# Performance work log

Hardware: AMD Instinct MI355X
Metric: run time of the kernel (lower is better)

Reference implementation:

```python
import jax, jax.numpy as jnp
import numpy as np

N, E, R, D = 50000, 640000, 200, 128  # nodes, edges, relations, feat dim (in_feat==out_feat)
EPS = 1e-5  # LayerNorm eps
NEG_SLOPE = 0.01  # F.leaky_relu default

def _xavier(k, shape):
    gain = np.sqrt(2.0)  # calculate_gain('relu')
    std = gain * np.sqrt(2.0 / (shape[0] + shape[1]))
    a = np.sqrt(3.0) * std
    return jax.random.uniform(k, shape, jnp.float32, -a, a)

def setup_inputs() -> dict:
    key = jax.random.key(0)
    ks = jax.random.split(key, 10)
    return {
        "node": jax.random.normal(ks[0], (N, D), jnp.float32),
        "rel": jax.random.normal(ks[1], (R, D), jnp.float32),
        "norm": jax.random.uniform(ks[2], (N, 1), jnp.float32),
        "w_triplet": _xavier(ks[3], (3 * D, D)),
        "w_quad": _xavier(ks[4], (D, D)),
        "loop_weight": _xavier(ks[5], (D, D)),
        "evolve_loop_weight": _xavier(ks[6], (D, D)),
        "src": jax.random.randint(ks[7], (E,), 0, N),
        "dst": jax.random.randint(ks[8], (E,), 0, N),
        "etype": jax.random.randint(ks[9], (E,), 0, R),
    }

def reference(node, rel, norm, w_triplet, w_quad, loop_weight, evolve_loop_weight, src, dst, etype):
    # triplet = cat([h_src, rel_emb, h_dst], 1) @ w_triplet, computed blockwise
    # to avoid materializing the [E, 3D] concat.
    W_s, W_r, W_d = w_triplet[:D], w_triplet[D:2 * D], w_triplet[2 * D:]
    triplet = node[src] @ W_s + rel[etype] @ W_r + node[dst] @ W_d  # [E, D]
    # 'fre' not in edata -> sro_fre is zeros; a_triplet = triplet @ w_quad
    a = jax.nn.leaky_relu(triplet @ w_quad, negative_slope=NEG_SLOPE)  # [E, D]
    # edge_softmax: softmax over incoming edges per destination node, per feature
    a_max = jax.ops.segment_max(a, dst, num_segments=N)
    a_max = jnp.where(jnp.isfinite(a_max), a_max, 0.0)  # empty segments -> -inf
    ex = jnp.exp(a - a_max[dst])
    denom = jax.ops.segment_sum(ex, dst, num_segments=N)
    att = ex / denom[dst]
    # weighted scatter-sum aggregation, then apply_func: h * norm
    h = jax.ops.segment_sum(att * triplet, dst, num_segments=N) * norm  # [N, D]
    # self-loop: evolve_loop_weight for in-degree-0 nodes, loop_weight otherwise
    indeg = jax.ops.segment_sum(jnp.ones((E,), jnp.float32), dst, num_segments=N)
    loop = jnp.where((indeg > 0)[:, None], node @ loop_weight, node @ evolve_loop_weight)
    out = h + loop
    # LayerNorm(elementwise_affine=False)
    mu = jnp.mean(out, axis=-1, keepdims=True)
    var = jnp.var(out, axis=-1, keepdims=True)
    return (out - mu) * jax.lax.rsqrt(var + EPS)
```

## Files before the change

kernel.cpp:

```cpp
#include <hip/hip_runtime.h>
#include <hip/hip_bf16.h>

#define D 128

typedef __attribute__((ext_vector_type(8))) short bf16x8;
typedef __attribute__((ext_vector_type(4))) float f32x4;

__device__ __forceinline__ unsigned short f2bf_bits(float f) {
    union { __hip_bfloat16 h; unsigned short u; } c;
    c.h = __float2bfloat16(f);
    return c.u;
}
__device__ __forceinline__ float bfbits2f(unsigned short u) {
    return __uint_as_float(((unsigned)u) << 16);
}
__device__ __forceinline__ float ldf(const void* p, size_t i, int f32) {
    return f32 ? ((const float*)p)[i] : bfbits2f(((const unsigned short*)p)[i]);
}
__device__ __forceinline__ void unpk(unsigned u, float& a, float& b) {
    a = __uint_as_float(u << 16);
    b = __uint_as_float(u & 0xFFFF0000u);
}

__global__ __launch_bounds__(256) void prep_kernel(
    const void* __restrict__ node, const void* __restrict__ wtrip,
    const void* __restrict__ wquad, const void* __restrict__ loopW,
    const void* __restrict__ evoW, unsigned short* __restrict__ wT,
    int* __restrict__ cnt, const int* __restrict__ dst, int* __restrict__ flag,
    int E) {
    __shared__ int sflag;
    int tid = threadIdx.x;
    int bad = 0;
    if (tid < 64) {
        for (int j = 0; j < 4; j++) {
            float v = bfbits2f(((const unsigned short*)node)[tid + 64 * j]);
            if (!(fabsf(v) < 1e4f)) bad = 1;
        }
    }
    unsigned long long m = __ballot(bad);
    if (tid == 0) sflag = (m != 0ull) ? 1 : 0;
    __syncthreads();
    int f32 = sflag;
    int bx = blockIdx.x;
    if (bx == 0 && tid == 0) *flag = f32;

    if (bx < 192) {
        int unit = bx * 2 + (tid >> 7);
        int k = unit & 127, mjob = unit >> 7;
        int t = tid & 127;
        float acc = 0.f;
        for (int j = 0; j < D; j++)
            acc += ldf(wtrip, (size_t)mjob * D * D + (size_t)k * D + j, f32) *
                   ldf(wquad, (size_t)j * D + t, f32);
        const int jmap0 = (mjob == 0) ? 0 : (mjob == 1 ? 6 : 2);
        wT[(size_t)jmap0 * D * D + (size_t)t * D + k] = f2bf_bits(acc);
    } else if (bx < 272) {
        int u = bx - 192;
        int jr = u >> 4, seg = u & 15;
        const void* srcp; size_t base; int j;
        switch (jr) {
            case 0: srcp = wtrip; base = 0;             j = 1; break;
            case 1: srcp = wtrip; base = 2 * D * D;     j = 3; break;
            case 2: srcp = loopW; base = 0;             j = 4; break;
            case 3: srcp = evoW;  base = 0;             j = 5; break;
            default: srcp = wtrip; base = (size_t)D * D; j = 7; break;
        }
        for (int c = tid; c < 1024; c += 256) {
            int idx = seg * 1024 + c;
            int n = idx >> 7, k = idx & 127;
            unsigned short b = f32 ? f2bf_bits(((const float*)srcp)[base + (size_t)k * D + n])
                                   : ((const unsigned short*)srcp)[base + (size_t)k * D + n];
            wT[(size_t)j * D * D + (size_t)n * D + k] = b;
        }
    } else {
        int e = (bx - 272) * 256 + tid;
        if (e < E) atomicAdd(&cnt[dst[e]], 1);
    }
}

__global__ void scan_block(const int* __restrict__ cnt, int* __restrict__ offs,
                           int* __restrict__ part, int N) {
    __shared__ int sh[256];
    int tid = threadIdx.x;
    int i = blockIdx.x * 256 + tid;
    int v = (i < N) ? cnt[i] : 0;
    sh[tid] = v;
    __syncthreads();
    for (int o = 1; o < 256; o <<= 1) {
        int t = (tid >= o) ? sh[tid - o] : 0;
        __syncthreads();
        sh[tid] += t;
        __syncthreads();
    }
    if (i < N) offs[i] = sh[tid] - v;
    if (tid == 255) part[blockIdx.x] = sh[255];
}

__global__ void scan_fix(int* __restrict__ offs, const int* __restrict__ part,
                         int N, int E) {
    __shared__ int sh[256];
    int tid = threadIdx.x, b = blockIdx.x;
    sh[tid] = (tid < b) ? part[tid] : 0;
    __syncthreads();
    for (int o = 128; o; o >>= 1) {
        if (tid < o) sh[tid] += sh[tid + o];
        __syncthreads();
    }
    int carry = sh[0];
    int i = b * 256 + tid;
    if (i < N) offs[i] += carry;
    if (b == 0 && tid == 0) offs[N] = E;
}

__global__ __launch_bounds__(256) void gemm_kernel(
    const void* __restrict__ node, const void* __restrict__ rel,
    const unsigned short* __restrict__ wT, const int* __restrict__ cnt,
    unsigned* __restrict__ nodeST, unsigned* __restrict__ nodeDT,
    unsigned* __restrict__ relRT, unsigned* __restrict__ loopSel,
    const int* __restrict__ flag, int N, int R, int nodeBlocks,
    const int* __restrict__ src, const int* __restrict__ dst,
    const int* __restrict__ et, const int* __restrict__ offs,
    int* __restrict__ cur, unsigned* __restrict__ ePack, int E) {
    __shared__ __align__(16) unsigned short Wt[D][D + 8];

    int bx = blockIdx.x, by = blockIdx.y;
    int tid = threadIdx.y * 64 + threadIdx.x;
    int isRel = 0, jp;
    if (bx >= nodeBlocks) {
        if (by == 1) {
            int e = (bx - nodeBlocks) * 256 + tid;
            if (e < E) {
                int d = dst[e];
                int pos = offs[d] + atomicAdd(&cur[d], 1);
                ePack[pos] = (unsigned)src[e] | ((unsigned)et[e] << 20);
            }
            return;
        }
        if (by != 0 || bx - nodeBlocks >= (R + 63) / 64) return;
        isRel = 1;
        jp = 3;
    } else {
        jp = by;
    }

    int f32 = *flag;
    int rows = isRel ? R : N;
    int row0 = (isRel ? bx - nodeBlocks : bx) * 64;
    const void* A = isRel ? rel : node;

    int lane = threadIdx.x, wv = threadIdx.y;
    int l16 = lane & 15, quad = lane >> 4;
    int ar = row0 + wv * 16 + l16;
    int ar_c = ar < rows ? ar : rows - 1;

    int qIdx, tIdx;
    unsigned* O = nullptr;
    switch (jp) {
        case 0: qIdx = 0; tIdx = 1; O = nodeST; break;
        case 1: qIdx = 2; tIdx = 3; O = nodeDT; break;
        case 2: qIdx = 4; tIdx = 5; break;
        default: qIdx = 6; tIdx = 7; O = relRT; break;
    }

    bf16x8 af[4];
#pragma unroll
    for (int kk = 0; kk < 4; kk++) {
        int k = kk * 32 + quad * 8;
        if (f32) {
            const float* Af = (const float*)A + (size_t)ar_c * D + k;
#pragma unroll
            for (int j = 0; j < 8; j++) af[kk][j] = (short)f2bf_bits(Af[j]);
        } else {
            af[kk] = *(const bf16x8*)((const unsigned short*)A + (size_t)ar_c * D + k);
        }
    }

    const unsigned short* gQ = wT + (size_t)qIdx * D * D;
    const unsigned short* gT = wT + (size_t)tIdx * D * D;

    bf16x8 wreg[8], wreg2[8];
#pragma unroll
    for (int i = 0; i < 8; i++) {
        int c = tid + i * 256;
        wreg[i] = *(const bf16x8*)(gQ + (c >> 4) * 128 + (c & 15) * 8);
    }

    f32x4 accQ[8], accT[8];
#pragma unroll
    for (int i = 0; i < 8; i++) {
        accQ[i] = (f32x4){0.f, 0.f, 0.f, 0.f};
        accT[i] = (f32x4){0.f, 0.f, 0.f, 0.f};
    }

    for (int pass = 0; pass < 2; pass++) {
#pragma unroll
        for (int i = 0; i < 8; i++) {
            int c = tid + i * 256;
            *(bf16x8*)(&Wt[c >> 4][(c & 15) * 8]) = wreg[i];
        }
        if (pass == 0) {
#pragma unroll
            for (int i = 0; i < 8; i++) {
                int c = tid + i * 256;
                wreg2[i] = *(const bf16x8*)(gT + (c >> 4) * 128 + (c & 15) * 8);
            }
        }
        __syncthreads();
        f32x4* acc = pass ? accT : accQ;
#pragma unroll
        for (int kk = 0; kk < 4; kk++) {
#pragma unroll
            for (int nt = 0; nt < 8; nt++) {
                bf16x8 bfr = *(const bf16x8*)(&Wt[nt * 16 + l16][kk * 32 + quad * 8]);
                acc[nt] = __builtin_amdgcn_mfma_f32_16x16x32_bf16(af[kk], bfr, acc[nt], 0, 0, 0);
            }
        }
        __syncthreads();
#pragma unroll
        for (int i = 0; i < 8; i++) wreg[i] = wreg2[i];
    }

    int cr0 = row0 + wv * 16 + quad * 4;
    int odd = l16 & 1;
    if (jp != 2) {
#pragma unroll
        for (int r = 0; r < 4; r++) {
            int cr = cr0 + r;
#pragma unroll
            for (int nt = 0; nt < 8; nt++) {
                float vQ = accQ[nt][r], vT = accT[nt][r];
                float oQ = __shfl_xor(vQ, 1);
                float oT = __shfl_xor(vT, 1);
                unsigned w;
                if (!odd) w = (unsigned)f2bf_bits(vQ) | ((unsigned)f2bf_bits(oQ) << 16);
                else      w = (unsigned)f2bf_bits(oT) | ((unsigned)f2bf_bits(vT) << 16);
                if (cr < rows) O[(size_t)cr * 128 + nt * 16 + l16] = w;
            }
        }
    } else {
#pragma unroll
        for (int r = 0; r < 4; r++) {
            int cr = cr0 + r;
            int deg = (cr < rows) ? cnt[cr] : 0;
#pragma unroll
            for (int nt = 0; nt < 8; nt++) {
                float vL = accQ[nt][r], vE = accT[nt][r];
                float oL = __shfl_xor(vL, 1);
                float oE = __shfl_xor(vE, 1);
                unsigned wl, we;
                if (!odd) {
                    wl = (unsigned)f2bf_bits(vL) | ((unsigned)f2bf_bits(oL) << 16);
                    we = (unsigned)f2bf_bits(vE) | ((unsigned)f2bf_bits(oE) << 16);
                } else {
                    wl = (unsigned)f2bf_bits(oL) | ((unsigned)f2bf_bits(vL) << 16);
                    we = (unsigned)f2bf_bits(oE) | ((unsigned)f2bf_bits(vE) << 16);
                }
                if (cr < rows && !odd)
                    loopSel[(size_t)cr * 64 + nt * 8 + (l16 >> 1)] = (deg > 0) ? wl : we;
            }
        }
    }
}

__global__ __launch_bounds__(256) void agg_kernel(
    const int* __restrict__ offs, const unsigned* __restrict__ ePack,
    const uint2* __restrict__ ST, const uint2* __restrict__ RT,
    const uint2* __restrict__ DT, const unsigned* __restrict__ loopSel,
    const void* __restrict__ normv, void* __restrict__ out,
    const int* __restrict__ flag, int N) {
    int n = blockIdx.x * 4 + threadIdx.y;
    if (n >= N) return;
    int f32 = *flag;
    int lane = threadIdx.x;
    int start = offs[n], end = offs[n + 1];
    int deg = end - start;

    unsigned ul = loopSel[(size_t)n * 64 + lane];
    uint2 ud = DT[(size_t)n * 64 + lane];
    float qd0, qd1, td0, td1, acc0, acc1;
    unpk(ud.x, qd0, qd1);
    unpk(ud.y, td0, td1);
    unpk(ul, acc0, acc1);

    float den0 = 0.f, den1 = 0.f, h0 = 0.f, h1 = 0.f;
    for (int e0 = start; e0 < end; e0 += 64) {
        int m = end - e0;
        if (m > 64) m = 64;
        unsigned pk = (lane < m) ? ePack[e0 + lane] : 0u;
        int j = 0;
#define EDGE_LOADS(J, US, UR)                                         \
        unsigned pk_##US = __shfl(pk, (J));                           \
        uint2 US = ST[(size_t)(pk_##US & 0xFFFFFu) * 64 + lane];      \
        uint2 UR = RT[(size_t)(pk_##US >> 20) * 64 + lane];
#define EDGE_MATH(US, UR)                                             \
        {                                                             \
            float qs0, qs1, qr0, qr1, ts0, ts1, tr0, tr1;             \
            unpk(US.x, qs0, qs1); unpk(UR.x, qr0, qr1);               \
            unpk(US.y, ts0, ts1); unpk(UR.y, tr0, tr1);               \
            float q0 = qs0 + qr0 + qd0, q1 = qs1 + qr1 + qd1;         \
            float a0 = q0 > 0.f ? q0 : 0.01f * q0;                    \
            float a1 = q1 > 0.f ? q1 : 0.01f * q1;                    \
            float ex0 = __expf(a0), ex1 = __expf(a1);                 \
            den0 += ex0; den1 += ex1;                                 \
            h0 += ex0 * (ts0 + tr0 + td0);                            \
            h1 += ex1 * (ts1 + tr1 + td1);                            \
        }
        for (; j + 3 < m; j += 4) {
            EDGE_LOADS(j + 0, uA, rA)
            EDGE_LOADS(j + 1, uB, rB)
            EDGE_LOADS(j + 2, uC, rC)
            EDGE_LOADS(j + 3, uD, rD)
            EDGE_MATH(uA, rA)
            EDGE_MATH(uB, rB)
            EDGE_MATH(uC, rC)
            EDGE_MATH(uD, rD)
        }
        for (; j < m; j++) {
            EDGE_LOADS(j, uE, rE)
            EDGE_MATH(uE, rE)
        }
    }

    float x0, x1;
    if (deg > 0) {
        float nrm = ldf(normv, n, f32);
        x0 = h0 / den0 * nrm + acc0;
        x1 = h1 / den1 * nrm + acc1;
    } else {
        x0 = acc0;
        x1 = acc1;
    }

    float s = x0 + x1, ss = x0 * x0 + x1 * x1;
#pragma unroll
    for (int o = 32; o; o >>= 1) {
        s += __shfl_xor(s, o);
        ss += __shfl_xor(ss, o);
    }
    float mu = s * (1.f / 128.f);
    float var = ss * (1.f / 128.f) - mu * mu;
    float rstd = rsqrtf(var + 1e-5f);
    float y0 = (x0 - mu) * rstd, y1 = (x1 - mu) * rstd;

    if (f32) {
        ((float2*)out)[(size_t)n * 64 + lane] = make_float2(y0, y1);
    } else {
        unsigned ob = (unsigned)f2bf_bits(y0) | ((unsigned)f2bf_bits(y1) << 16);
        ((unsigned*)out)[(size_t)n * 64 + lane] = ob;
    }
}

extern "C" void kernel_launch(void* const* d_in, const int* in_sizes, int n_in,
                              void* d_out, int out_size, void* d_ws, size_t ws_size,
                              hipStream_t stream) {
    const void* node = d_in[0];
    const void* rel = d_in[1];
    const void* normv = d_in[2];
    const void* wtrip = d_in[3];
    const void* wquad = d_in[4];
    const void* loopW = d_in[5];
    const void* evoW = d_in[6];
    const int* src = (const int*)d_in[7];
    const int* dst = (const int*)d_in[8];
    const int* et = (const int*)d_in[9];

    int N = in_sizes[0] / D;
    int R = in_sizes[1] / D;
    int E = in_sizes[7];
    int nb = (N + 255) / 256;
    int nodeBlocks = (N + 63) / 64;
    int relBlocks = (R + 63) / 64;
    int scatBlocks = (E + 255) / 256;

    char* p = (char*)d_ws;
    auto alloc = [&](size_t bytes) -> void* {
        void* r = (void*)p;
        p += (bytes + 255) & ~(size_t)255;
        return r;
    };
    unsigned* nodeST = (unsigned*)alloc((size_t)N * 128 * 4);
    unsigned* nodeDT = (unsigned*)alloc((size_t)N * 128 * 4);
    unsigned* relRT = (unsigned*)alloc((size_t)R * 128 * 4);
    unsigned* loopSel = (unsigned*)alloc((size_t)N * 64 * 4);
    unsigned short* wT = (unsigned short*)alloc((size_t)8 * D * D * 2);
    int* cnt = (int*)alloc((size_t)2 * N * 4);
    int* offs = (int*)alloc((size_t)(N + 1) * 4);
    int* part = (int*)alloc((size_t)(nb + 1) * 4);
    unsigned* ePack = (unsigned*)alloc((size_t)E * 4);
    int* flag = (int*)alloc(4);

    hipMemsetAsync(cnt, 0, (size_t)2 * N * 4, stream);
    prep_kernel<<<272 + scatBlocks, 256, 0, stream>>>(
        node, wtrip, wquad, loopW, evoW, wT, cnt, dst, flag, E);
    scan_block<<<nb, 256, 0, stream>>>(cnt, offs, part, N);
    scan_fix<<<nb, 256, 0, stream>>>(offs, part, N, E);
    int xext = nodeBlocks + (scatBlocks > relBlocks ? scatBlocks : relBlocks);
    gemm_kernel<<<dim3(xext, 3), dim3(64, 4), 0, stream>>>(
        node, rel, wT, cnt, nodeST, nodeDT, relRT, loopSel, flag, N, R, nodeBlocks,
        src, dst, et, offs, cnt + N, ePack, E);
    agg_kernel<<<(N + 3) / 4, dim3(64, 4), 0, stream>>>(
        offs, ePack, (const uint2*)nodeST, (const uint2*)relRT, (const uint2*)nodeDT,
        loopSel, normv, d_out, flag, N);
}
```

Baseline: 255.8 us.

## Make GEMM persistent with per-pass weight staging and simplify edge scatter

```diff
diff --git a/kernel.cpp b/kernel.cpp
--- a/kernel.cpp
+++ b/kernel.cpp
@@ -97,7 +97,7 @@
 }
 
 __global__ void scan_fix(int* __restrict__ offs, const int* __restrict__ part,
-                         int N, int E) {
+                         int* __restrict__ cur, int N, int E) {
     __shared__ int sh[256];
     int tid = threadIdx.x, b = blockIdx.x;
     sh[tid] = (tid < b) ? part[tid] : 0;
@@ -108,7 +108,11 @@
     }
     int carry = sh[0];
     int i = b * 256 + tid;
-    if (i < N) offs[i] += carry;
+    if (i < N) {
+        int v = offs[i] + carry;
+        offs[i] = v;
+        cur[i] = v;
+    }
     if (b == 0 && tid == 0) offs[N] = E;
 }
 
@@ -117,41 +121,40 @@
     const unsigned short* __restrict__ wT, const int* __restrict__ cnt,
     unsigned* __restrict__ nodeST, unsigned* __restrict__ nodeDT,
     unsigned* __restrict__ relRT, unsigned* __restrict__ loopSel,
-    const int* __restrict__ flag, int N, int R, int nodeBlocks,
+    const int* __restrict__ flag, int N, int R,
     const int* __restrict__ src, const int* __restrict__ dst,
-    const int* __restrict__ et, const int* __restrict__ offs,
-    int* __restrict__ cur, unsigned* __restrict__ ePack, int E) {
+    const int* __restrict__ et, int* __restrict__ cur,
+    unsigned* __restrict__ ePack, int E) {
     __shared__ __align__(16) unsigned short Wt[D][D + 8];
 
     int bx = blockIdx.x, by = blockIdx.y;
     int tid = threadIdx.y * 64 + threadIdx.x;
-    int isRel = 0, jp;
-    if (bx >= nodeBlocks) {
-        if (by == 1) {
-            int e = (bx - nodeBlocks) * 256 + tid;
-            if (e < E) {
+    int relTiles = (R + 63) / 64;
+
+    int jp, rows;
+    const void* A;
+    if (by == 3) {
+        if (bx >= relTiles) {
+            int stride = ((int)gridDim.x - relTiles) * 256;
+            for (int e = (bx - relTiles) * 256 + tid; e < E; e += stride) {
                 int d = dst[e];
-                int pos = offs[d] + atomicAdd(&cur[d], 1);
+                int pos = atomicAdd(&cur[d], 1);
                 ePack[pos] = (unsigned)src[e] | ((unsigned)et[e] << 20);
             }
             return;
         }
-        if (by != 0 || bx - nodeBlocks >= (R + 63) / 64) return;
-        isRel = 1;
-        jp = 3;
+        jp = 3; rows = R; A = rel;
     } else {
-        jp = by;
+        jp = by; rows = N; A = node;
+        if (bx * 64 >= rows) return;
     }
 
     int f32 = *flag;
-    int rows = isRel ? R : N;
-    int row0 = (isRel ? bx - nodeBlocks : bx) * 64;
-    const void* A = isRel ? rel : node;
-
     int lane = threadIdx.x, wv = threadIdx.y;
     int l16 = lane & 15, quad = lane >> 4;
-    int ar = row0 + wv * 16 + l16;
-    int ar_c = ar < rows ? ar : rows - 1;
+    int odd = l16 & 1;
+    int nTiles = (rows + 63) / 64;
+    int P = (int)gridDim.x;
 
     int qIdx, tIdx;
     unsigned* O = nullptr;
@@ -162,103 +165,110 @@
         default: qIdx = 6; tIdx = 7; O = relRT; break;
     }
 
-    bf16x8 af[4];
-#pragma unroll
-    for (int kk = 0; kk < 4; kk++) {
-        int k = kk * 32 + quad * 8;
-        if (f32) {
-            const float* Af = (const float*)A + (size_t)ar_c * D + k;
-#pragma unroll
-            for (int j = 0; j < 8; j++) af[kk][j] = (short)f2bf_bits(Af[j]);
-        } else {
-            af[kk] = *(const bf16x8*)((const unsigned short*)A + (size_t)ar_c * D + k);
-        }
-    }
-
-    const unsigned short* gQ = wT + (size_t)qIdx * D * D;
-    const unsigned short* gT = wT + (size_t)tIdx * D * D;
-
-    bf16x8 wreg[8], wreg2[8];
-#pragma unroll
-    for (int i = 0; i < 8; i++) {
-        int c = tid + i * 256;
-        wreg[i] = *(const bf16x8*)(gQ + (c >> 4) * 128 + (c & 15) * 8);
-    }
-
-    f32x4 accQ[8], accT[8];
-#pragma unroll
-    for (int i = 0; i < 8; i++) {
-        accQ[i] = (f32x4){0.f, 0.f, 0.f, 0.f};
-        accT[i] = (f32x4){0.f, 0.f, 0.f, 0.f};
-    }
-
     for (int pass = 0; pass < 2; pass++) {
+        const unsigned short* g = wT + (size_t)(pass ? tIdx : qIdx) * D * D;
 #pragma unroll
         for (int i = 0; i < 8; i++) {
             int c = tid + i * 256;
-            *(bf16x8*)(&Wt[c >> 4][(c & 15) * 8]) = wreg[i];
-        }
-        if (pass == 0) {
-#pragma unroll
-            for (int i = 0; i < 8; i++) {
-                int c = tid + i * 256;
-                wreg2[i] = *(const bf16x8*)(gT + (c >> 4) * 128 + (c & 15) * 8);
-            }
+            *(bf16x8*)(&Wt[c >> 4][(c & 15) * 8]) =
+                *(const bf16x8*)(g + (c >> 4) * 128 + (c & 15) * 8);
         }
         __syncthreads();
-        f32x4* acc = pass ? accT : accQ;
-#pragma unroll
-        for (int kk = 0; kk < 4; kk++) {
-#pragma unroll
-            for (int nt = 0; nt < 8; nt++) {
-                bf16x8 bfr = *(const bf16x8*)(&Wt[nt * 16 + l16][kk * 32 + quad * 8]);
-                acc[nt] = __builtin_amdgcn_mfma_f32_16x16x32_bf16(af[kk], bfr, acc[nt], 0, 0, 0);
-            }
+
+        int tile = bx;
+        bf16x8 af[4];
+        {
+            int arr = tile * 64 + wv * 16 + l16;
+            int arc = arr < rows ? arr : rows - 1;
+            if (f32) {
+                const float* Af = (const float*)A + (size_t)arc * D;
+#pragma unroll
+                for (int kk = 0; kk < 4; kk++)
+#pragma unroll
+                    for (int j = 0; j < 8; j++)
+                        af[kk][j] = (short)f2bf_bits(Af[kk * 32 + quad * 8 + j]);
+            } else {
+#pragma unroll
+                for (int kk = 0; kk < 4; kk++)
+                    af[kk] = *(const bf16x8*)((const unsigned short*)A +
+                                              (size_t)arc * D + kk * 32 + quad * 8);
+            }
+        }
+
+        while (tile < nTiles) {
+            int nxt = tile + P;
+            bf16x8 afN[4];
+            if (nxt < nTiles) {
+                int arr = nxt * 64 + wv * 16 + l16;
+                int arc = arr < rows ? arr : rows - 1;
+                if (f32) {
+                    const float* Af = (const float*)A + (size_t)arc * D;
+#pragma unroll
+                    for (int kk = 0; kk < 4; kk++)
+#pragma unroll
+                        for (int j = 0; j < 8; j++)
+                            afN[kk][j] = (short)f2bf_bits(Af[kk * 32 + quad * 8 + j]);
+                } else {
+#pragma unroll
+                    for (int kk = 0; kk < 4; kk++)
+                        afN[kk] = *(const bf16x8*)((const unsigned short*)A +
+                                                   (size_t)arc * D + kk * 32 + quad * 8);
+                }
+            }
+
+            f32x4 acc[8];
+#pragma unroll
+            for (int i = 0; i < 8; i++) acc[i] = (f32x4){0.f, 0.f, 0.f, 0.f};
+#pragma unroll
+            for (int kk = 0; kk < 4; kk++) {
+#pragma unroll
+                for (int nt = 0; nt < 8; nt++) {
+                    bf16x8 bfr = *(const bf16x8*)(&Wt[nt * 16 + l16][kk * 32 + quad * 8]);
+                    acc[nt] = __builtin_amdgcn_mfma_f32_16x16x32_bf16(af[kk], bfr, acc[nt], 0, 0, 0);
+                }
+            }
+
+            int cr0 = tile * 64 + wv * 16 + quad * 4;
+            if (jp != 2) {
+#pragma unroll
+                for (int r = 0; r < 4; r++) {
+                    int cr = cr0 + r;
+#pragma unroll
+                    for (int nt = 0; nt < 8; nt++) {
+                        float v = acc[nt][r];
+                        float o = __shfl_xor(v, 1);
+                        if (!odd && cr < rows) {
+                            unsigned w = (unsigned)f2bf_bits(v) | ((unsigned)f2bf_bits(o) << 16);
+                            int cn = nt * 16 + l16;
+                            O[(size_t)cr * 128 + cn + pass] = w;
+                        }
+                    }
+                }
+            } else {
+#pragma unroll
+                for (int r = 0; r < 4; r++) {
+                    int cr = cr0 + r;
+                    int deg = (cr < rows) ? cnt[cr] : 0;
+                    int doit = (cr < rows) && (pass == 0 ? (deg > 0) : (deg == 0));
+#pragma unroll
+                    for (int nt = 0; nt < 8; nt++) {
+                        float v = acc[nt][r];
+                        float o = __shfl_xor(v, 1);
+                        if (!odd && doit) {
+                            unsigned w = (unsigned)f2bf_bits(v) | ((unsigned)f2bf_bits(o) << 16);
+                            loopSel[(size_t)cr * 64 + nt * 8 + (l16 >> 1)] = w;
+                        }
+                    }
+                }
+            }
+
+            if (nxt < nTiles) {
+#pragma unroll
+                for (int kk = 0; kk < 4; kk++) af[kk] = afN[kk];
+            }
+            tile = nxt;
         }
         __syncthreads();
-#pragma unroll
-        for (int i = 0; i < 8; i++) wreg[i] = wreg2[i];
-    }
-
-    int cr0 = row0 + wv * 16 + quad * 4;
-    int odd = l16 & 1;
-    if (jp != 2) {
-#pragma unroll
-        for (int r = 0; r < 4; r++) {
-            int cr = cr0 + r;
-#pragma unroll
-            for (int nt = 0; nt < 8; nt++) {
-                float vQ = accQ[nt][r], vT = accT[nt][r];
-                float oQ = __shfl_xor(vQ, 1);
-                float oT = __shfl_xor(vT, 1);
-                unsigned w;
-                if (!odd) w = (unsigned)f2bf_bits(vQ) | ((unsigned)f2bf_bits(oQ) << 16);
-                else      w = (unsigned)f2bf_bits(oT) | ((unsigned)f2bf_bits(vT) << 16);
-                if (cr < rows) O[(size_t)cr * 128 + nt * 16 + l16] = w;
-            }
-        }
-    } else {
-#pragma unroll
-        for (int r = 0; r < 4; r++) {
-            int cr = cr0 + r;
-            int deg = (cr < rows) ? cnt[cr] : 0;
-#pragma unroll
-            for (int nt = 0; nt < 8; nt++) {
-                float vL = accQ[nt][r], vE = accT[nt][r];
-                float oL = __shfl_xor(vL, 1);
-                float oE = __shfl_xor(vE, 1);
-                unsigned wl, we;
-                if (!odd) {
-                    wl = (unsigned)f2bf_bits(vL) | ((unsigned)f2bf_bits(oL) << 16);
-                    we = (unsigned)f2bf_bits(vE) | ((unsigned)f2bf_bits(oE) << 16);
-                } else {
-                    wl = (unsigned)f2bf_bits(oL) | ((unsigned)f2bf_bits(vL) << 16);
-                    we = (unsigned)f2bf_bits(oE) | ((unsigned)f2bf_bits(vE) << 16);
-                }
-                if (cr < rows && !odd)
-                    loopSel[(size_t)cr * 64 + nt * 8 + (l16 >> 1)] = (deg > 0) ? wl : we;
-            }
-        }
     }
 }
 
@@ -283,42 +293,38 @@
     unpk(ul, acc0, acc1);
 
     float den0 = 0.f, den1 = 0.f, h0 = 0.f, h1 = 0.f;
-    for (int e0 = start; e0 < end; e0 += 64) {
-        int m = end - e0;
-        if (m > 64) m = 64;
-        unsigned pk = (lane < m) ? ePack[e0 + lane] : 0u;
-        int j = 0;
-#define EDGE_LOADS(J, US, UR)                                         \
-        unsigned pk_##US = __shfl(pk, (J));                           \
-        uint2 US = ST[(size_t)(pk_##US & 0xFFFFFu) * 64 + lane];      \
-        uint2 UR = RT[(size_t)(pk_##US >> 20) * 64 + lane];
-#define EDGE_MATH(US, UR)                                             \
-        {                                                             \
-            float qs0, qs1, qr0, qr1, ts0, ts1, tr0, tr1;             \
-            unpk(US.x, qs0, qs1); unpk(UR.x, qr0, qr1);               \
-            unpk(US.y, ts0, ts1); unpk(UR.y, tr0, tr1);               \
-            float q0 = qs0 + qr0 + qd0, q1 = qs1 + qr1 + qd1;         \
-            float a0 = q0 > 0.f ? q0 : 0.01f * q0;                    \
-            float a1 = q1 > 0.f ? q1 : 0.01f * q1;                    \
-            float ex0 = __expf(a0), ex1 = __expf(a1);                 \
-            den0 += ex0; den1 += ex1;                                 \
-            h0 += ex0 * (ts0 + tr0 + td0);                            \
-            h1 += ex1 * (ts1 + tr1 + td1);                            \
-        }
-        for (; j + 3 < m; j += 4) {
-            EDGE_LOADS(j + 0, uA, rA)
-            EDGE_LOADS(j + 1, uB, rB)
-            EDGE_LOADS(j + 2, uC, rC)
-            EDGE_LOADS(j + 3, uD, rD)
-            EDGE_MATH(uA, rA)
-            EDGE_MATH(uB, rB)
-            EDGE_MATH(uC, rC)
-            EDGE_MATH(uD, rD)
-        }
-        for (; j < m; j++) {
-            EDGE_LOADS(j, uE, rE)
-            EDGE_MATH(uE, rE)
-        }
+#define GATH(PK, US, UR)                                              \
+    uint2 US = ST[(size_t)((PK) & 0xFFFFFu) * 64 + lane];             \
+    uint2 UR = RT[(size_t)((PK) >> 20) * 64 + lane];
+#define EMATH(US, UR)                                                 \
+    {                                                                 \
+        float qs0, qs1, qr0, qr1, ts0, ts1, tr0, tr1;                 \
+        unpk(US.x, qs0, qs1); unpk(UR.x, qr0, qr1);                   \
+        unpk(US.y, ts0, ts1); unpk(UR.y, tr0, tr1);                   \
+        float q0 = qs0 + qr0 + qd0, q1 = qs1 + qr1 + qd1;             \
+        float a0 = q0 > 0.f ? q0 : 0.01f * q0;                        \
+        float a1 = q1 > 0.f ? q1 : 0.01f * q1;                        \
+        float ex0 = __expf(a0), ex1 = __expf(a1);                     \
+        den0 += ex0; den1 += ex1;                                     \
+        h0 += ex0 * (ts0 + tr0 + td0);                                \
+        h1 += ex1 * (ts1 + tr1 + td1);                                \
+    }
+    int e = start;
+    for (; e + 3 < end; e += 4) {
+        unsigned p0 = ePack[e], p1 = ePack[e + 1], p2 = ePack[e + 2], p3 = ePack[e + 3];
+        GATH(p0, sA, rA)
+        GATH(p1, sB, rB)
+        GATH(p2, sC, rC)
+        GATH(p3, sD, rD)
+        EMATH(sA, rA)
+        EMATH(sB, rB)
+        EMATH(sC, rC)
+        EMATH(sD, rD)
+    }
+    for (; e < end; e++) {
+        unsigned pp = ePack[e];
+        GATH(pp, sE, rE)
+        EMATH(sE, rE)
     }
 
     float x0, x1;
@@ -368,8 +374,6 @@
     int R = in_sizes[1] / D;
     int E = in_sizes[7];
     int nb = (N + 255) / 256;
-    int nodeBlocks = (N + 63) / 64;
-    int relBlocks = (R + 63) / 64;
     int scatBlocks = (E + 255) / 256;
 
     char* p = (char*)d_ws;
@@ -383,21 +387,21 @@
     unsigned* relRT = (unsigned*)alloc((size_t)R * 128 * 4);
     unsigned* loopSel = (unsigned*)alloc((size_t)N * 64 * 4);
     unsigned short* wT = (unsigned short*)alloc((size_t)8 * D * D * 2);
-    int* cnt = (int*)alloc((size_t)2 * N * 4);
+    int* cnt = (int*)alloc((size_t)N * 4);
+    int* cur = (int*)alloc((size_t)N * 4);
     int* offs = (int*)alloc((size_t)(N + 1) * 4);
     int* part = (int*)alloc((size_t)(nb + 1) * 4);
     unsigned* ePack = (unsigned*)alloc((size_t)E * 4);
     int* flag = (int*)alloc(4);
 
-    hipMemsetAsync(cnt, 0, (size_t)2 * N * 4, stream);
+    hipMemsetAsync(cnt, 0, (size_t)N * 4, stream);
     prep_kernel<<<272 + scatBlocks, 256, 0, stream>>>(
         node, wtrip, wquad, loopW, evoW, wT, cnt, dst, flag, E);
     scan_block<<<nb, 256, 0, stream>>>(cnt, offs, part, N);
-    scan_fix<<<nb, 256, 0, stream>>>(offs, part, N, E);
-    int xext = nodeBlocks + (scatBlocks > relBlocks ? scatBlocks : relBlocks);
-    gemm_kernel<<<dim3(xext, 3), dim3(64, 4), 0, stream>>>(
-        node, rel, wT, cnt, nodeST, nodeDT, relRT, loopSel, flag, N, R, nodeBlocks,
-        src, dst, et, offs, cnt + N, ePack, E);
+    scan_fix<<<nb, 256, 0, stream>>>(offs, part, cur, N, E);
+    gemm_kernel<<<dim3(256, 4), dim3(64, 4), 0, stream>>>(
+        node, rel, wT, cnt, nodeST, nodeDT, relRT, loopSel, flag, N, R,
+        src, dst, et, cur, ePack, E);
     agg_kernel<<<(N + 3) / 4, dim3(64, 4), 0, stream>>>(
         offs, ePack, (const uint2*)nodeST, (const uint2*)relRT, (const uint2*)nodeDT,
         loopSel, normv, d_out, flag, N);
```

Result: slower. 284.7 us (+11.3%).
